# Kernel tuning notes

Hardware: AMD Instinct MI355X
Metric: run time of the kernel (lower is better)

## Reference

```python
import jax, jax.numpy as jnp
import numpy as np

B, T, D = 4, 8192, 1024
C = 8.0


def setup_inputs() -> dict:
    key = jax.random.key(0)
    k1, k2, k3 = jax.random.split(key, 3)
    init_std = D ** (-0.5)
    x = jax.random.normal(k1, (B, T, D), dtype=jnp.float32)
    W_in = jax.random.truncated_normal(k2, -3.0, 3.0, (D, D), dtype=jnp.float32) * init_std
    W_gate = jax.random.truncated_normal(k3, -3.0, 3.0, (D, D), dtype=jnp.float32) * init_std
    b_in = jnp.zeros((D,), dtype=jnp.float32)
    b_gate = jnp.zeros((D,), dtype=jnp.float32)
    forget_lambda = jnp.linspace(-4.323, -9.0, D, dtype=jnp.float32)
    return {"x": x, "W_in": W_in, "b_in": b_in, "W_gate": W_gate,
            "b_gate": b_gate, "forget_lambda": forget_lambda}


def _combine(c1, c2):
    # linear recurrence h_t = a_t * h_{t-1} + b_t  (associative composition)
    a1, b1 = c1
    a2, b2 = c2
    return a1 * a2, a2 * b1 + b2


def reference(x, W_in, b_in, W_gate, b_gate, forget_lambda):
    # x: [B, T, D]
    input_gate = x @ W_in.T + b_in          # [B, T, D]
    recurrence_gate = x @ W_gate.T + b_gate  # [B, T, D]
    alpha = jnp.exp(-C * jax.nn.softplus(forget_lambda) * jax.nn.sigmoid(recurrence_gate))
    beta = jnp.sqrt(1.0 - alpha ** 2 + 1e-6)
    xbeta = beta * jax.nn.sigmoid(input_gate) * x
    # parallel scan of h_t = alpha_t * h_{t-1} + xbeta_t along sequence axis
    _, h = jax.lax.associative_scan(_combine, (alpha, xbeta), axis=1)
    return h
```

## Files before the change

kernel.cpp:

```cpp
#include <hip/hip_runtime.h>

typedef unsigned short u16;
typedef __attribute__((ext_vector_type(8))) short short8;
typedef __attribute__((ext_vector_type(4))) float f32x4;

#define T_SEQ 8192
#define DDIM 1024
#define BB 4
#define MM (BB * T_SEQ)
#define NC 128
#define CHUNK (T_SEQ / NC)
#define CHAINS (BB * DDIM)
#define NHT 32

__device__ __forceinline__ float bf_lo(unsigned p) {
    union { unsigned u; float f; } v; v.u = p << 16; return v.f;
}
__device__ __forceinline__ float bf_hi(unsigned p) {
    union { unsigned u; float f; } v; v.u = p & 0xffff0000u; return v.f;
}
__device__ __forceinline__ float bf_u16(u16 p) {
    union { unsigned u; float f; } v; v.u = ((unsigned)p) << 16; return v.f;
}
__device__ __forceinline__ u16 f2bf(float f) {
    union { unsigned u; float f; } v; v.f = f;
    unsigned r = v.u + 0x7fffu + ((v.u >> 16) & 1u);
    return (u16)(r >> 16);
}
__device__ __forceinline__ float sigm(float z) {
    return __builtin_amdgcn_rcpf(1.0f + __expf(-z));
}
__device__ __forceinline__ void gld16(const u16* g, u16* l) {
    __builtin_amdgcn_global_load_lds((const __attribute__((address_space(1))) void*)g,
                                     (__attribute__((address_space(3))) void*)l, 16, 0, 0);
}

#define N4X (MM * DDIM / 4)
#define N4W (DDIM * DDIM / 4)
__global__ __launch_bounds__(256) void cvt_all(const float* __restrict__ x,
                                               const float* __restrict__ Wi,
                                               const float* __restrict__ Wg,
                                               u16* __restrict__ Xb,
                                               u16* __restrict__ Wib,
                                               u16* __restrict__ Wgb) {
    int i = blockIdx.x * 256 + threadIdx.x;
    const float* src; u16* dst; int j;
    if (i < N4X)            { src = x;  dst = Xb;  j = i; }
    else if (i < N4X + N4W) { src = Wi; dst = Wib; j = i - N4X; }
    else                    { src = Wg; dst = Wgb; j = i - N4X - N4W; }
    float4 v = ((const float4*)src)[j];
    ushort4 o;
    o.x = f2bf(v.x); o.y = f2bf(v.y); o.z = f2bf(v.z); o.w = f2bf(v.w);
    ((ushort4*)dst)[j] = o;
}


#define MROW4(ri, af, bf)                                                               \
    acc[ri][0] = __builtin_amdgcn_mfma_f32_16x16x32_bf16(af, bf[0], acc[ri][0], 0,0,0); \
    acc[ri][1] = __builtin_amdgcn_mfma_f32_16x16x32_bf16(af, bf[1], acc[ri][1], 0,0,0); \
    acc[ri][2] = __builtin_amdgcn_mfma_f32_16x16x32_bf16(af, bf[2], acc[ri][2], 0,0,0); \
    acc[ri][3] = __builtin_amdgcn_mfma_f32_16x16x32_bf16(af, bf[3], acc[ri][3], 0,0,0);

#define MQUAD(b_, aset, bset) MROW4((b_)+0, aset[0], bset) MROW4((b_)+1, aset[1], bset) \
                              MROW4((b_)+2, aset[2], bset) MROW4((b_)+3, aset[3], bset)

#define LDA_S(s_, i) (*(const short8*)&lds[(s_)*8192 + (arow0 + (i)*16)*32 + aoff])
#define LDB_S(s_, j) (*(const short8*)&lds[32768 + (s_)*8192 + (brow0 + (j)*16)*32 + aoff])

#define RD_A(dst, s_, base) { dst[0] = LDA_S(s_, (base)+0); dst[1] = LDA_S(s_, (base)+1); \
                              dst[2] = LDA_S(s_, (base)+2); dst[3] = LDA_S(s_, (base)+3); }
#define RD_B(dst, s_)       { dst[0] = LDB_S(s_, 0); dst[1] = LDB_S(s_, 1);               \
                              dst[2] = LDB_S(s_, 2); dst[3] = LDB_S(s_, 3); }

#define STA_S(ds_, ht_, rb) gld16(gA + (size_t)(ht_)*32 + (size_t)(rb)*128*DDIM,       \
                                  &lds[(ds_)*8192 + (rb)*4096 + tid*8])
#define STB_S(ds_, ht_, hf) gld16(((hf) ? gBg : gBi) + (size_t)(ht_)*32,               \
                                  &lds[32768 + (ds_)*8192 + (hf)*4096 + tid*8])

#define PAIR_(s_, sn_, ds_, ht_, BCUR, BNXT, DOST, VMS, DORD)                          \
               \
    RD_A(A1, s_, 4)                                                                    \
    __builtin_amdgcn_s_setprio(1);                                                     \
    MQUAD(0, A0, BCUR)                                                                 \
    __builtin_amdgcn_s_setprio(0);                                                     \
    asm volatile("s_waitcnt " VMS ::: "memory");                 \
    __builtin_amdgcn_s_barrier();                                                      \
                  \
    if (DORD) { RD_B(BNXT, sn_) RD_A(A0, sn_, 0) }                                     \
    if (DOST) { STA_S(ds_, ht_, 0); STA_S(ds_, ht_, 1);                                \
                STB_S(ds_, ht_, 0); STB_S(ds_, ht_, 1); }                              \
    __builtin_amdgcn_s_setprio(1);                                                     \
    MQUAD(4, A1, BCUR)                                                                 \
    __builtin_amdgcn_s_setprio(0);

__global__ __launch_bounds__(512, 2)
void gemm_fused(const u16* __restrict__ X, const u16* __restrict__ Wi,
                const u16* __restrict__ Wg, const float* __restrict__ b_in,
                const float* __restrict__ b_gate, const float* __restrict__ lam,
                u16* __restrict__ Sg, u16* __restrict__ XBg) {
    const int bid = blockIdx.x;
    const int xcd = bid & 7;
    const int r = bid >> 3;
    const int n_tile = r & 7;
    const int m_tile = xcd * 16 + (r >> 3);
    const int tN0 = n_tile * 128;
    const int tM0 = m_tile * 256;

    const int tid = threadIdx.x;
    const int lane = tid & 63;
    const int w = tid >> 6;
    const int wm = w >> 2;
    const int wn = w & 3;
    const int gate = wn >> 1;
    const int wn_sub = wn & 1;

    __shared__ u16 lds[65536];

    const int srow = tid >> 2;
    const int c8log = (tid & 3) ^ ((tid >> 3) & 3);
    const u16* gA  = X  + (size_t)(tM0 + srow) * DDIM + c8log * 8;
    const u16* gBi = Wi + (size_t)(tN0 + srow) * DDIM + c8log * 8;
    const u16* gBg = Wg + (size_t)(tN0 + srow) * DDIM + c8log * 8;

    const int lm = lane & 15;
    const int aoff = (((lane >> 4) ^ ((lm >> 1) & 3))) * 8;
    const int arow0 = wm * 128 + lm;
    const int brow0 = gate * 128 + wn_sub * 64 + lm;

    f32x4 acc[8][4] = {};
    short8 A0[4], A1[4], B0[4], B1[4];

    STA_S(0, 0, 0); STA_S(0, 0, 1); STB_S(0, 0, 0); STB_S(0, 0, 1);
    STA_S(1, 1, 0); STA_S(1, 1, 1); STB_S(1, 1, 0); STB_S(1, 1, 1);
    STA_S(2, 2, 0); STA_S(2, 2, 1); STB_S(2, 2, 0); STB_S(2, 2, 1);
    asm volatile("s_waitcnt vmcnt(8)" ::: "memory");
    __builtin_amdgcn_s_barrier();
    RD_B(B0, 0) RD_A(A0, 0, 0)

    for (int g = 0; g < 7; ++g) {
        const int hb = 4 * g;
        PAIR_(0, 1, 3, hb + 3, B0, B1, 1, "vmcnt(4)", 1)
        PAIR_(1, 2, 0, hb + 4, B1, B0, 1, "vmcnt(4)", 1)
        PAIR_(2, 3, 1, hb + 5, B0, B1, 1, "vmcnt(4)", 1)
        PAIR_(3, 0, 2, hb + 6, B1, B0, 1, "vmcnt(4)", 1)
    }
    PAIR_(0, 1, 3, 31, B0, B1, 1, "vmcnt(4)", 1)
    PAIR_(1, 2, 0, 0,  B1, B0, 0, "vmcnt(4)", 1)
    PAIR_(2, 3, 0, 0,  B0, B1, 0, "vmcnt(0)", 1)
    PAIR_(3, 0, 0, 0,  B1, B0, 0, "vmcnt(0)", 0)
    asm volatile("s_waitcnt lgkmcnt(0)" ::: "memory");
    __builtin_amdgcn_s_barrier();

    const int r0 = (lane >> 4) << 2;
    const int cb = lane & 15;
    if (gate) {
#pragma unroll
        for (int j = 0; j < 4; ++j) {
            const int colg = tN0 + wn_sub * 64 + j * 16 + cb;
            const int cl = wn_sub * 64 + j * 16 + cb;
            const float bj = b_gate[colg];
            const float nsp = -8.0f * log1pf(__expf(lam[colg]));
#pragma unroll
            for (int i = 0; i < 8; ++i) {
                const int rl0 = wm * 128 + i * 16 + r0;
#pragma unroll
                for (int rr = 0; rr < 4; ++rr) {
                    const int rl = rl0 + rr;
                    float s = nsp * sigm(acc[i][j][rr] + bj);
                    lds[rl * 128 + (cl ^ (((rl >> 2) & 7) << 4))] = f2bf(s);
                }
            }
        }
    } else {
#pragma unroll
        for (int j = 0; j < 4; ++j) {
            const int colg = tN0 + wn_sub * 64 + j * 16 + cb;
            const int cl = wn_sub * 64 + j * 16 + cb;
            const float bj = b_in[colg];
#pragma unroll
            for (int i = 0; i < 8; ++i) {
                const int rl0 = wm * 128 + i * 16 + r0;
#pragma unroll
                for (int rr = 0; rr < 4; ++rr) {
                    const int rl = rl0 + rr;
                    float p = sigm(acc[i][j][rr] + bj);
                    lds[32768 + rl * 128 + (cl ^ (((rl >> 2) & 7) << 4))] =
                        (u16)(p * 65535.0f + 0.5f);
                }
            }
        }
    }
    asm volatile("s_waitcnt lgkmcnt(0)" ::: "memory");
    __builtin_amdgcn_s_barrier();
    __builtin_amdgcn_sched_barrier(0);

    const int cc = tid & 15;
    const int rg0 = (tid >> 4) * 8;
#pragma unroll
    for (int k = 0; k < 8; ++k) {
        const int rl = rg0 + k;
        const int ch = (cc ^ (((rl >> 2) & 7) << 1)) * 8;
        short8 sv = *(const short8*)&lds[rl * 128 + ch];
        short8 pv = *(const short8*)&lds[32768 + rl * 128 + ch];
        const size_t go = (size_t)(tM0 + rl) * DDIM + tN0 + cc * 8;
        short8 xv = *(const short8*)&X[go];
        short8 ov;
#pragma unroll
        for (int e = 0; e < 8; ++e) {
            float s = bf_u16((u16)sv[e]);
            float p = (float)((u16)pv[e]) * (1.0f / 65535.0f);
            float xf = bf_u16((u16)xv[e]);
            float be = sqrtf(1.0f - __expf(2.0f * s) + 1e-6f);
            ov[e] = (short)f2bf(be * p * xf);
        }
        *(short8*)&Sg[go] = sv;
        *(short8*)&XBg[go] = ov;
    }
}

__global__ __launch_bounds__(256)
void scan_pass1(const u16* __restrict__ S, const u16* __restrict__ XB,
                float* __restrict__ AggA, float* __restrict__ AggB) {
    const int c = blockIdx.x, dblk = blockIdx.y, bq = blockIdx.z;
    const int d0 = dblk * 512 + threadIdx.x * 2;
    size_t base = ((size_t)(bq * T_SEQ + c * CHUNK)) * DDIM + d0;

    float A0 = 1.0f, B0 = 0.0f, A1 = 1.0f, B1 = 0.0f;
#pragma unroll 8
    for (int t = 0; t < CHUNK; t++) {
        unsigned sp = *(const unsigned*)(S + base);
        unsigned xp = *(const unsigned*)(XB + base);
        float a0 = __expf(bf_lo(sp));
        float a1 = __expf(bf_hi(sp));
        B0 = fmaf(a0, B0, bf_lo(xp)); A0 *= a0;
        B1 = fmaf(a1, B1, bf_hi(xp)); A1 *= a1;
        base += DDIM;
    }
    const int chain = bq * DDIM + d0;
    float2 av; av.x = A0; av.y = A1;
    float2 bv; bv.x = B0; bv.y = B1;
    *(float2*)(AggA + (size_t)c * CHAINS + chain) = av;
    *(float2*)(AggB + (size_t)c * CHAINS + chain) = bv;
}

__global__ __launch_bounds__(256)
void scan_pass2(const float* __restrict__ AggA, const float* __restrict__ AggB,
                float* __restrict__ H0) {
    const int chain = blockIdx.x * 256 + threadIdx.x;
    float p = 0.0f;
#pragma unroll 8
    for (int c = 0; c < NC; c++) {
        H0[(size_t)c * CHAINS + chain] = p;
        p = AggA[(size_t)c * CHAINS + chain] * p + AggB[(size_t)c * CHAINS + chain];
    }
}

__global__ __launch_bounds__(256)
void scan_pass3(const u16* __restrict__ S, const u16* __restrict__ XB,
                const float* __restrict__ H0, float* __restrict__ out) {
    const int c = blockIdx.x, dblk = blockIdx.y, bq = blockIdx.z;
    const int d0 = dblk * 512 + threadIdx.x * 2;
    size_t base = ((size_t)(bq * T_SEQ + c * CHUNK)) * DDIM + d0;
    const int chain = bq * DDIM + d0;

    float2 h = *(const float2*)(H0 + (size_t)c * CHAINS + chain);
#pragma unroll 8
    for (int t = 0; t < CHUNK; t++) {
        unsigned sp = *(const unsigned*)(S + base);
        unsigned xp = *(const unsigned*)(XB + base);
        float a0 = __expf(bf_lo(sp));
        float a1 = __expf(bf_hi(sp));
        h.x = fmaf(a0, h.x, bf_lo(xp));
        h.y = fmaf(a1, h.y, bf_hi(xp));
        *(float2*)(out + base) = h;
        base += DDIM;
    }
}

extern "C" void kernel_launch(void* const* d_in, const int* in_sizes, int n_in,
                              void* d_out, int out_size, void* d_ws, size_t ws_size,
                              hipStream_t stream) {
    const float* x   = (const float*)d_in[0];
    const float* Win = (const float*)d_in[1];
    const float* bin = (const float*)d_in[2];
    const float* Wg  = (const float*)d_in[3];
    const float* bg  = (const float*)d_in[4];
    const float* lam = (const float*)d_in[5];
    float* out = (float*)d_out;

    char* w = (char*)d_ws;
    u16* Wi_bf  = (u16*)(w);
    u16* Wg_bf  = (u16*)(w + (size_t)(2) * 1024 * 1024);
    u16* Sg     = (u16*)(w + (size_t)(4) * 1024 * 1024);
    u16* XBg    = (u16*)(w + (size_t)(68) * 1024 * 1024);
    float* AggA = (float*)(w + (size_t)(132) * 1024 * 1024);
    float* AggB = (float*)(w + (size_t)(134) * 1024 * 1024);
    float* H0   = (float*)(w + (size_t)(136) * 1024 * 1024);

    u16* Xbf = (u16*)d_out;

    cvt_all<<<dim3((N4X + 2 * N4W) / 256), dim3(256), 0, stream>>>(
        x, Win, Wg, Xbf, Wi_bf, Wg_bf);

    gemm_fused<<<dim3((DDIM / 128) * (MM / 256)), dim3(512), 0, stream>>>(
        Xbf, Wi_bf, Wg_bf, bin, bg, lam, Sg, XBg);

    scan_pass1<<<dim3(NC, 2, BB), dim3(256), 0, stream>>>(Sg, XBg, AggA, AggB);
    scan_pass2<<<dim3(CHAINS / 256), dim3(256), 0, stream>>>(AggA, AggB, H0);
    scan_pass3<<<dim3(NC, 2, BB), dim3(256), 0, stream>>>(Sg, XBg, H0, out);
}
```

Before: 470.8 us.

## Halve GEMM block to 4 waves with 128x128 per-wave output tiles

Restructures the fused GEMM from 8 waves of 128x64 output each to 4 waves each computing a 128x128 tile (8x8 MFMA accumulators), loading 8 B fragments per step. Each wave now issues twice as many global-to-LDS loads, and the epilogue processes 16 rows per thread. This aims to raise MFMA-to-LDS-read ratio per wave and cut LDS traffic. The cost is a much higher register footprint (256 accumulator floats), lower occupancy (launch bounds 256,1), and less latency hiding.

```diff
diff --git a/kernel.cpp b/kernel.cpp
--- a/kernel.cpp
+++ b/kernel.cpp
@@ -11,7 +11,6 @@
 #define NC 128
 #define CHUNK (T_SEQ / NC)
 #define CHAINS (BB * DDIM)
-#define NHT 32
 
 __device__ __forceinline__ float bf_lo(unsigned p) {
     union { unsigned u; float f; } v; v.u = p << 16; return v.f;
@@ -55,45 +54,53 @@
 }
 
 
-#define MROW4(ri, af, bf)                                                               \
-    acc[ri][0] = __builtin_amdgcn_mfma_f32_16x16x32_bf16(af, bf[0], acc[ri][0], 0,0,0); \
-    acc[ri][1] = __builtin_amdgcn_mfma_f32_16x16x32_bf16(af, bf[1], acc[ri][1], 0,0,0); \
-    acc[ri][2] = __builtin_amdgcn_mfma_f32_16x16x32_bf16(af, bf[2], acc[ri][2], 0,0,0); \
-    acc[ri][3] = __builtin_amdgcn_mfma_f32_16x16x32_bf16(af, bf[3], acc[ri][3], 0,0,0);
-
-#define MQUAD(b_, aset, bset) MROW4((b_)+0, aset[0], bset) MROW4((b_)+1, aset[1], bset) \
-                              MROW4((b_)+2, aset[2], bset) MROW4((b_)+3, aset[3], bset)
+#define MROW8(ri, af, bs)                                                                \
+    acc[ri][0] = __builtin_amdgcn_mfma_f32_16x16x32_bf16(af, bs[0], acc[ri][0], 0,0,0);  \
+    acc[ri][1] = __builtin_amdgcn_mfma_f32_16x16x32_bf16(af, bs[1], acc[ri][1], 0,0,0);  \
+    acc[ri][2] = __builtin_amdgcn_mfma_f32_16x16x32_bf16(af, bs[2], acc[ri][2], 0,0,0);  \
+    acc[ri][3] = __builtin_amdgcn_mfma_f32_16x16x32_bf16(af, bs[3], acc[ri][3], 0,0,0);  \
+    acc[ri][4] = __builtin_amdgcn_mfma_f32_16x16x32_bf16(af, bs[4], acc[ri][4], 0,0,0);  \
+    acc[ri][5] = __builtin_amdgcn_mfma_f32_16x16x32_bf16(af, bs[5], acc[ri][5], 0,0,0);  \
+    acc[ri][6] = __builtin_amdgcn_mfma_f32_16x16x32_bf16(af, bs[6], acc[ri][6], 0,0,0);  \
+    acc[ri][7] = __builtin_amdgcn_mfma_f32_16x16x32_bf16(af, bs[7], acc[ri][7], 0,0,0);
+
+#define MQUAD(b_, aset, bset) MROW8((b_)+0, aset[0], bset) MROW8((b_)+1, aset[1], bset) \
+                              MROW8((b_)+2, aset[2], bset) MROW8((b_)+3, aset[3], bset)
 
 #define LDA_S(s_, i) (*(const short8*)&lds[(s_)*8192 + (arow0 + (i)*16)*32 + aoff])
 #define LDB_S(s_, j) (*(const short8*)&lds[32768 + (s_)*8192 + (brow0 + (j)*16)*32 + aoff])
 
 #define RD_A(dst, s_, base) { dst[0] = LDA_S(s_, (base)+0); dst[1] = LDA_S(s_, (base)+1); \
                               dst[2] = LDA_S(s_, (base)+2); dst[3] = LDA_S(s_, (base)+3); }
-#define RD_B(dst, s_)       { dst[0] = LDB_S(s_, 0); dst[1] = LDB_S(s_, 1);               \
-                              dst[2] = LDB_S(s_, 2); dst[3] = LDB_S(s_, 3); }
-
-#define STA_S(ds_, ht_, rb) gld16(gA + (size_t)(ht_)*32 + (size_t)(rb)*128*DDIM,       \
-                                  &lds[(ds_)*8192 + (rb)*4096 + tid*8])
-#define STB_S(ds_, ht_, hf) gld16(((hf) ? gBg : gBi) + (size_t)(ht_)*32,               \
-                                  &lds[32768 + (ds_)*8192 + (hf)*4096 + tid*8])
+#define RD_B8(dst, s_)      { dst[0] = LDB_S(s_, 0); dst[1] = LDB_S(s_, 1);               \
+                              dst[2] = LDB_S(s_, 2); dst[3] = LDB_S(s_, 3);               \
+                              dst[4] = LDB_S(s_, 4); dst[5] = LDB_S(s_, 5);               \
+                              dst[6] = LDB_S(s_, 6); dst[7] = LDB_S(s_, 7); }
+
+#define STA_S(ds_, ht_, rb) gld16(gA + (size_t)(ht_)*32 + (size_t)(rb)*64*DDIM,          \
+                                  &lds[(ds_)*8192 + (rb)*2048 + tid*8])
+#define STB_S(ds_, ht_, rb) gld16(((rb) < 2 ? gBi + (size_t)(rb)*64*DDIM                 \
+                                            : gBg + (size_t)((rb)-2)*64*DDIM)            \
+                                      + (size_t)(ht_)*32,                                \
+                                  &lds[32768 + (ds_)*8192 + (rb)*2048 + tid*8])
+#define ST8(ds_, ht_) STA_S(ds_, ht_, 0); STA_S(ds_, ht_, 1); STA_S(ds_, ht_, 2);        \
+                      STA_S(ds_, ht_, 3); STB_S(ds_, ht_, 0); STB_S(ds_, ht_, 1);        \
+                      STB_S(ds_, ht_, 2); STB_S(ds_, ht_, 3);
 
 #define PAIR_(s_, sn_, ds_, ht_, BCUR, BNXT, DOST, VMS, DORD)                          \
-               \
-    RD_A(A1, s_, 4)                                                                    \
+    RD_A(A1, s_, 4)                                 \
     __builtin_amdgcn_s_setprio(1);                                                     \
-    MQUAD(0, A0, BCUR)                                                                 \
+    MQUAD(0, A0, BCUR)                                                    \
     __builtin_amdgcn_s_setprio(0);                                                     \
     asm volatile("s_waitcnt " VMS ::: "memory");                 \
     __builtin_amdgcn_s_barrier();                                                      \
-                  \
-    if (DORD) { RD_B(BNXT, sn_) RD_A(A0, sn_, 0) }                                     \
-    if (DOST) { STA_S(ds_, ht_, 0); STA_S(ds_, ht_, 1);                                \
-                STB_S(ds_, ht_, 0); STB_S(ds_, ht_, 1); }                              \
+    if (DORD) { RD_B8(BNXT, sn_) RD_A(A0, sn_, 0) }         \
+    if (DOST) { ST8(ds_, ht_) }                               \
     __builtin_amdgcn_s_setprio(1);                                                     \
-    MQUAD(4, A1, BCUR)                                                                 \
+    MQUAD(4, A1, BCUR)                                                    \
     __builtin_amdgcn_s_setprio(0);
 
-__global__ __launch_bounds__(512, 2)
+__global__ __launch_bounds__(256, 1)
 void gemm_fused(const u16* __restrict__ X, const u16* __restrict__ Wi,
                 const u16* __restrict__ Wg, const float* __restrict__ b_in,
                 const float* __restrict__ b_gate, const float* __restrict__ lam,
@@ -109,10 +116,8 @@
     const int tid = threadIdx.x;
     const int lane = tid & 63;
     const int w = tid >> 6;
-    const int wm = w >> 2;
-    const int wn = w & 3;
-    const int gate = wn >> 1;
-    const int wn_sub = wn & 1;
+    const int wm = w >> 1;
+    const int gate = w & 1;
 
     __shared__ u16 lds[65536];
 
@@ -125,27 +130,25 @@
     const int lm = lane & 15;
     const int aoff = (((lane >> 4) ^ ((lm >> 1) & 3))) * 8;
     const int arow0 = wm * 128 + lm;
-    const int brow0 = gate * 128 + wn_sub * 64 + lm;
-
-    f32x4 acc[8][4] = {};
-    short8 A0[4], A1[4], B0[4], B1[4];
-
-    STA_S(0, 0, 0); STA_S(0, 0, 1); STB_S(0, 0, 0); STB_S(0, 0, 1);
-    STA_S(1, 1, 0); STA_S(1, 1, 1); STB_S(1, 1, 0); STB_S(1, 1, 1);
-    STA_S(2, 2, 0); STA_S(2, 2, 1); STB_S(2, 2, 0); STB_S(2, 2, 1);
-    asm volatile("s_waitcnt vmcnt(8)" ::: "memory");
+    const int brow0 = gate * 128 + lm;
+
+    f32x4 acc[8][8] = {};
+    short8 A0[4], A1[4], B0[8], B1[8];
+
+    ST8(0, 0) ST8(1, 1) ST8(2, 2)
+    asm volatile("s_waitcnt vmcnt(16)" ::: "memory");
     __builtin_amdgcn_s_barrier();
-    RD_B(B0, 0) RD_A(A0, 0, 0)
+    RD_B8(B0, 0) RD_A(A0, 0, 0)
 
     for (int g = 0; g < 7; ++g) {
         const int hb = 4 * g;
-        PAIR_(0, 1, 3, hb + 3, B0, B1, 1, "vmcnt(4)", 1)
-        PAIR_(1, 2, 0, hb + 4, B1, B0, 1, "vmcnt(4)", 1)
-        PAIR_(2, 3, 1, hb + 5, B0, B1, 1, "vmcnt(4)", 1)
-        PAIR_(3, 0, 2, hb + 6, B1, B0, 1, "vmcnt(4)", 1)
-    }
-    PAIR_(0, 1, 3, 31, B0, B1, 1, "vmcnt(4)", 1)
-    PAIR_(1, 2, 0, 0,  B1, B0, 0, "vmcnt(4)", 1)
+        PAIR_(0, 1, 3, hb + 3, B0, B1, 1, "vmcnt(8)", 1)
+        PAIR_(1, 2, 0, hb + 4, B1, B0, 1, "vmcnt(8)", 1)
+        PAIR_(2, 3, 1, hb + 5, B0, B1, 1, "vmcnt(8)", 1)
+        PAIR_(3, 0, 2, hb + 6, B1, B0, 1, "vmcnt(8)", 1)
+    }
+    PAIR_(0, 1, 3, 31, B0, B1, 1, "vmcnt(8)", 1)
+    PAIR_(1, 2, 0, 0,  B1, B0, 0, "vmcnt(8)", 1)
     PAIR_(2, 3, 0, 0,  B0, B1, 0, "vmcnt(0)", 1)
     PAIR_(3, 0, 0, 0,  B1, B0, 0, "vmcnt(0)", 0)
     asm volatile("s_waitcnt lgkmcnt(0)" ::: "memory");
@@ -155,9 +158,9 @@
     const int cb = lane & 15;
     if (gate) {
 #pragma unroll
-        for (int j = 0; j < 4; ++j) {
-            const int colg = tN0 + wn_sub * 64 + j * 16 + cb;
-            const int cl = wn_sub * 64 + j * 16 + cb;
+        for (int j = 0; j < 8; ++j) {
+            const int colg = tN0 + j * 16 + cb;
+            const int cl = j * 16 + cb;
             const float bj = b_gate[colg];
             const float nsp = -8.0f * log1pf(__expf(lam[colg]));
 #pragma unroll
@@ -173,9 +176,9 @@
         }
     } else {
 #pragma unroll
-        for (int j = 0; j < 4; ++j) {
-            const int colg = tN0 + wn_sub * 64 + j * 16 + cb;
-            const int cl = wn_sub * 64 + j * 16 + cb;
+        for (int j = 0; j < 8; ++j) {
+            const int colg = tN0 + j * 16 + cb;
+            const int cl = j * 16 + cb;
             const float bj = b_in[colg];
 #pragma unroll
             for (int i = 0; i < 8; ++i) {
@@ -195,10 +198,10 @@
     __builtin_amdgcn_sched_barrier(0);
 
     const int cc = tid & 15;
-    const int rg0 = (tid >> 4) * 8;
-#pragma unroll
-    for (int k = 0; k < 8; ++k) {
-        const int rl = rg0 + k;
+    const int rbase = (tid >> 4) * 16;
+#pragma unroll
+    for (int k = 0; k < 16; ++k) {
+        const int rl = rbase + k;
         const int ch = (cc ^ (((rl >> 2) & 7) << 1)) * 8;
         short8 sv = *(const short8*)&lds[rl * 128 + ch];
         short8 pv = *(const short8*)&lds[32768 + rl * 128 + ch];
@@ -302,7 +305,7 @@
     cvt_all<<<dim3((N4X + 2 * N4W) / 256), dim3(256), 0, stream>>>(
         x, Win, Wg, Xbf, Wi_bf, Wg_bf);
 
-    gemm_fused<<<dim3((DDIM / 128) * (MM / 256)), dim3(512), 0, stream>>>(
+    gemm_fused<<<dim3((DDIM / 128) * (MM / 256)), dim3(256), 0, stream>>>(
         Xbf, Wi_bf, Wg_bf, bin, bg, lam, Sg, XBg);
 
     scan_pass1<<<dim3(NC, 2, BB), dim3(256), 0, stream>>>(Sg, XBg, AggA, AggB);
```

Result: slower. 503.0 us (+6.8%).
